# Kernel optimization log

Measured on AMD Instinct MI355X. Metric: run time of the kernel, lower is better.

Reference implementation:

```python
import jax, jax.numpy as jnp
import numpy as np

B, S, D, H = 4, 2048, 768, 12
HD = D // H
SCALE = HD ** -0.5


def setup_inputs() -> dict:
    key = jax.random.key(0)
    ks = jax.random.split(key, 10)
    inp = {
        "x": jax.random.normal(ks[0], (B, S, D), jnp.float32),
        "attn_mask": jax.random.normal(ks[1], (B, S), jnp.float32),
        "Wq": jax.random.normal(ks[2], (D, D), jnp.float32) * (D ** -0.5),
        "bq": jax.random.normal(ks[3], (D,), jnp.float32) * 0.02,
        "Wk": jax.random.normal(ks[4], (D, D), jnp.float32) * (D ** -0.5),
        "bk": jax.random.normal(ks[5], (D,), jnp.float32) * 0.02,
        "Wv": jax.random.normal(ks[6], (D, D), jnp.float32) * (D ** -0.5),
        "bv": jax.random.normal(ks[7], (D,), jnp.float32) * 0.02,
        "Wo": jax.random.normal(ks[8], (D, D), jnp.float32) * (D ** -0.5),
        "bo": jax.random.normal(ks[9], (D,), jnp.float32) * 0.02,
    }
    return inp


def _split_heads(e):
    # [B, S, D] -> [B, H, S, HD]
    return e.reshape(B, S, H, HD).transpose(0, 2, 1, 3)


def reference(x, attn_mask, Wq, bq, Wk, bk, Wv, bv, Wo, bo):
    q = _split_heads((x @ Wq + bq) * SCALE)          # [B,H,S,HD]
    k = _split_heads(x @ Wk + bk)                     # [B,H,S,HD]
    v = _split_heads(x @ Wv + bv)                     # [B,H,S,HD]
    scores = jnp.einsum('bhsd,bhtd->bhst', q, k)      # [B,H,S,S]
    scores = scores + attn_mask[:, None, None, :]     # additive mask over keys
    probs = jax.nn.softmax(scores, axis=-1)
    out = jnp.einsum('bhst,bhtd->bhsd', probs, v)     # [B,H,S,HD]
    out = out.transpose(0, 2, 1, 3).reshape(B, S, D)  # merge heads
    return out @ Wo + bo
```

## Files before the change

### kernel.cpp

```cpp
#include <hip/hip_runtime.h>
#include <cmath>

#define B_ 4
#define S_ 2048
#define D_ 768
#define H_ 12
#define HD_ 64
#define SCALE_ 0.125f
#define LOG2E_ 1.4426950408889634f
#define M_ 8192
#define NE_ 6291456ull

typedef unsigned short ushortT;
typedef unsigned int u32;
typedef __attribute__((ext_vector_type(8))) __bf16 bf16x8;
typedef __attribute__((ext_vector_type(4))) float f32x4;
typedef __attribute__((ext_vector_type(16))) float f32x16;

typedef __attribute__((address_space(1))) const void glb_cv;
typedef __attribute__((address_space(3))) void lds_v;

__device__ inline ushortT f2bf(float f) {
    return __builtin_bit_cast(ushortT, (__bf16)f);
}

__device__ inline u32 pk2bf(float a, float b) {
    return (u32)__builtin_bit_cast(ushortT, (__bf16)a)
         | ((u32)__builtin_bit_cast(ushortT, (__bf16)b) << 16);
}

__device__ inline void gload_lds16(const void* g, void* l) {
    __builtin_amdgcn_global_load_lds((glb_cv*)g, (lds_v*)l, 16, 0, 0);
}

__global__ __launch_bounds__(256)
void convert_f32_bf16(const float* __restrict__ in, ushortT* __restrict__ out)
{
    const size_t i = ((size_t)blockIdx.x * 256 + threadIdx.x) * 8;
    float4 a = *(const float4*)(in + i);
    float4 b = *(const float4*)(in + i + 4);
    union { ushortT u[8]; float4 f; } o;
    o.u[0] = f2bf(a.x); o.u[1] = f2bf(a.y); o.u[2] = f2bf(a.z); o.u[3] = f2bf(a.w);
    o.u[4] = f2bf(b.x); o.u[5] = f2bf(b.y); o.u[6] = f2bf(b.z); o.u[7] = f2bf(b.w);
    *(float4*)(out + i) = o.f;
}

__global__ __launch_bounds__(256)
void scale_mask(const float* __restrict__ in, float* __restrict__ outp)
{
    const int i = blockIdx.x * 256 + threadIdx.x;
    outp[i] = in[i] * LOG2E_;
}

__global__ __launch_bounds__(256)
void transpose_w(const float* __restrict__ W0, const float* __restrict__ W1,
                 const float* __restrict__ W2, const float* __restrict__ W3,
                 ushortT* __restrict__ wt4)
{
    const float* W = (blockIdx.z == 0) ? W0 : (blockIdx.z == 1) ? W1
                   : (blockIdx.z == 2) ? W2 : W3;
    ushortT* o = wt4 + (size_t)blockIdx.z * 768 * 768;
    __shared__ float T[64][65];
    const int tid = threadIdx.x;
    const int k0 = blockIdx.x * 64, n0 = blockIdx.y * 64;

    for (int t = tid; t < 1024; t += 256) {
        const int r = t >> 4, c4 = (t & 15) << 2;
        float4 v = *(const float4*)&W[(size_t)(k0 + r) * 768 + n0 + c4];
        T[r][c4 + 0] = v.x; T[r][c4 + 1] = v.y;
        T[r][c4 + 2] = v.z; T[r][c4 + 3] = v.w;
    }
    __syncthreads();
    for (int t = tid; t < 1024; t += 256) {
        const int r = t >> 4, c4 = (t & 15) << 2;
        union { ushortT u[4]; unsigned long long v; } ov;
        ov.u[0] = f2bf(T[c4 + 0][r]); ov.u[1] = f2bf(T[c4 + 1][r]);
        ov.u[2] = f2bf(T[c4 + 2][r]); ov.u[3] = f2bf(T[c4 + 3][r]);
        *(unsigned long long*)&o[(size_t)(n0 + r) * 768 + k0 + c4] = ov.v;
    }
}

__device__ inline void gemm_core_128x64(
    const ushortT* __restrict__ A, const ushortT* __restrict__ Bt,
    ushortT* As, ushortT* Bs, int m0, int n0, f32x4 acc[4][2])
{
    const int tid  = threadIdx.x;
    const int lane = tid & 63;
    const int wave = tid >> 6;
    const int lr = lane & 15, lg = lane >> 4;
    const int wr = wave >> 1, wc = wave & 1;

    #pragma unroll
    for (int mi = 0; mi < 4; ++mi)
        #pragma unroll
        for (int ni = 0; ni < 2; ++ni)
            acc[mi][ni] = (f32x4){0.f, 0.f, 0.f, 0.f};

    #pragma unroll 1
    for (int k0 = 0; k0 < 768; k0 += 64) {
        __syncthreads();
        #pragma unroll
        for (int it = 0; it < 4; ++it) {
            const int ci = it * 256 + tid;
            const int row = ci >> 3, c = ci & 7;
            const int sc = c ^ (row & 7);
            gload_lds16(A + (size_t)(m0 + row) * 768 + k0 + sc * 8,
                        As + (size_t)(it * 256 + wave * 64) * 8);
        }
        #pragma unroll
        for (int it = 0; it < 2; ++it) {
            const int ci = it * 256 + tid;
            const int row = ci >> 3, c = ci & 7;
            const int sc = c ^ (row & 7);
            gload_lds16(Bt + (size_t)(n0 + row) * 768 + k0 + sc * 8,
                        Bs + (size_t)(it * 256 + wave * 64) * 8);
        }
        __syncthreads();

        #pragma unroll
        for (int ks = 0; ks < 2; ++ks) {
            bf16x8 af[4], bfr[2];
            #pragma unroll
            for (int mi = 0; mi < 4; ++mi) {
                const int row = wr * 64 + mi * 16 + lr;
                const int ch = (ks * 4 + lg) ^ (row & 7);
                af[mi] = __builtin_bit_cast(bf16x8, *(const float4*)(As + row * 64 + ch * 8));
            }
            #pragma unroll
            for (int ni = 0; ni < 2; ++ni) {
                const int row = wc * 32 + ni * 16 + lr;
                const int ch = (ks * 4 + lg) ^ (row & 7);
                bfr[ni] = __builtin_bit_cast(bf16x8, *(const float4*)(Bs + row * 64 + ch * 8));
            }
            #pragma unroll
            for (int mi = 0; mi < 4; ++mi)
                #pragma unroll
                for (int ni = 0; ni < 2; ++ni)
                    acc[mi][ni] = __builtin_amdgcn_mfma_f32_16x16x32_bf16(
                        af[mi], bfr[ni], acc[mi][ni], 0, 0, 0);
        }
    }
}

__global__ __launch_bounds__(256)
void qkv_gemm(const ushortT* __restrict__ xb, const ushortT* __restrict__ wt4,
              const float* __restrict__ bq, const float* __restrict__ bk,
              const float* __restrict__ bv,
              ushortT* __restrict__ qb, ushortT* __restrict__ kb,
              ushortT* __restrict__ vtb)
{
    __shared__ __align__(16) ushortT As[128 * 64];
    __shared__ __align__(16) ushortT Bs[64 * 64];
    const int z = blockIdx.z;
    const ushortT* Wt = wt4 + (size_t)z * 768 * 768;
    const float* bias = (z == 0) ? bq : (z == 1) ? bk : bv;
    const float scale = (z == 0) ? (SCALE_ * LOG2E_) : 1.0f;

    const int m0 = blockIdx.x * 128, n0 = blockIdx.y * 64;
    f32x4 acc[4][2];
    gemm_core_128x64(xb, Wt, As, Bs, m0, n0, acc);

    const int tid = threadIdx.x;
    const int lane = tid & 63, wave = tid >> 6;
    const int lr = lane & 15, lg = lane >> 4;
    const int wr = wave >> 1, wc = wave & 1;
    const int h = n0 >> 6;

    if (z == 2) {
        #pragma unroll
        for (int ni = 0; ni < 2; ++ni) {
            const int nn = wc * 32 + ni * 16 + lr;
            const float bb = bias[n0 + nn];
            #pragma unroll
            for (int mi = 0; mi < 4; ++mi) {
                const int mb = m0 + wr * 64 + mi * 16 + lg * 4;
                const int b = mb >> 11, s = mb & 2047;
                ushort4 ov;
                ov.x = f2bf(acc[mi][ni][0] + bb);
                ov.y = f2bf(acc[mi][ni][1] + bb);
                ov.z = f2bf(acc[mi][ni][2] + bb);
                ov.w = f2bf(acc[mi][ni][3] + bb);
                *(ushort4*)&vtb[(((size_t)b * H_ + h) * HD_ + nn) * S_ + s] = ov;
            }
        }
    } else {
        ushortT* out = (z == 0) ? qb : kb;
        #pragma unroll
        for (int ni = 0; ni < 2; ++ni) {
            const int nn = wc * 32 + ni * 16 + lr;
            const float bb = bias[n0 + nn];
            #pragma unroll
            for (int mi = 0; mi < 4; ++mi) {
                #pragma unroll
                for (int j = 0; j < 4; ++j) {
                    const int m = m0 + wr * 64 + mi * 16 + lg * 4 + j;
                    const int b = m >> 11, s = m & 2047;
                    out[(((size_t)b * H_ + h) * S_ + s) * HD_ + nn] =
                        f2bf((acc[mi][ni][j] + bb) * scale);
                }
            }
        }
    }
}

__global__ __launch_bounds__(256)
void o_gemm(const ushortT* __restrict__ ab, const ushortT* __restrict__ wto,
            const float* __restrict__ bo, float* __restrict__ out)
{
    __shared__ __align__(16) ushortT As[128 * 64];
    __shared__ __align__(16) ushortT Bs[64 * 64];
    const int m0 = blockIdx.x * 128, n0 = blockIdx.y * 64;
    f32x4 acc[4][2];
    gemm_core_128x64(ab, wto, As, Bs, m0, n0, acc);

    const int tid = threadIdx.x;
    const int lane = tid & 63, wave = tid >> 6;
    const int lr = lane & 15, lg = lane >> 4;
    const int wr = wave >> 1, wc = wave & 1;

    #pragma unroll
    for (int ni = 0; ni < 2; ++ni) {
        const int n = n0 + wc * 32 + ni * 16 + lr;
        const float bb = bo[n];
        #pragma unroll
        for (int mi = 0; mi < 4; ++mi) {
            #pragma unroll
            for (int j = 0; j < 4; ++j) {
                const int m = m0 + wr * 64 + mi * 16 + lg * 4 + j;
                out[(size_t)m * 768 + n] = acc[mi][ni][j] + bb;
            }
        }
    }
}

__global__ __launch_bounds__(256, 3)
void attn_mfma(const ushortT* __restrict__ Q, const ushortT* __restrict__ K,
               const ushortT* __restrict__ Vt, const float* __restrict__ msc,
               ushortT* __restrict__ out)
{
    __shared__ __align__(16) ushortT Ks[2][64 * 64];
    __shared__ __align__(16) ushortT Vs[2][64 * 64];

    const int tid  = threadIdx.x;
    const int lane = tid & 63;
    const int wq   = tid >> 6;
    const int col  = lane & 31;
    const int hi   = lane >> 5;

    const int gid  = blockIdx.x;
    const int xcd  = gid & 7;
    const int w    = gid >> 3;
    const int bh_i = xcd * 6 + (w >> 4);
    const int q0   = (w & 15) * 128;
    const int b    = bh_i / H_;
    const int h    = bh_i % H_;
    const size_t bh = (size_t)bh_i;

    bf16x8 qf[4];
    {
        const ushortT* Qg = Q + (bh * S_ + q0 + wq * 32 + col) * HD_;
        #pragma unroll
        for (int ks = 0; ks < 4; ++ks)
            qf[ks] = __builtin_bit_cast(bf16x8,
                *(const float4*)(Qg + ks * 16 + hi * 8));
    }

    const ushortT* Kg = K  + bh * S_ * HD_;
    const ushortT* Vg = Vt + bh * HD_ * S_;
    const float*   mg = msc + (size_t)b * S_;

    const ushortT* ksrc[2];
    const ushortT* vsrc[2];
    #pragma unroll
    for (int it = 0; it < 2; ++it) {
        const int ci = it * 256 + tid;
        const int row = ci >> 3, c = ci & 7, sc = c ^ (row & 7);
        ksrc[it] = Kg + (size_t)row * HD_ + sc * 8;
        vsrc[it] = Vg + (size_t)row * S_ + sc * 8;
    }

    int ko[2][4], vo[2][4];
    #pragma unroll
    for (int kb2 = 0; kb2 < 2; ++kb2) {
        const int r = kb2 * 32 + col;
        #pragma unroll
        for (int ks = 0; ks < 4; ++ks)
            ko[kb2][ks] = r * 128 + (((2 * ks + hi) ^ (r & 7)) << 4);
    }
    #pragma unroll
    for (int hb = 0; hb < 2; ++hb) {
        const int r = hb * 32 + col;
        #pragma unroll
        for (int sg = 0; sg < 4; ++sg)
            vo[hb][sg] = r * 128 + (((2 * sg + hi) ^ (r & 7)) << 4);
    }

    bf16x8 onesA;
    #pragma unroll
    for (int i = 0; i < 8; ++i) onesA[i] = (__bf16)1.0f;

    f32x16 acc[2];
    f32x16 accl;
    #pragma unroll
    for (int hb = 0; hb < 2; ++hb)
        #pragma unroll
        for (int r = 0; r < 16; ++r) acc[hb][r] = 0.f;
    #pragma unroll
    for (int r = 0; r < 16; ++r) accl[r] = 0.f;

    auto stage = [&](int bsel) {
        #pragma unroll
        for (int it = 0; it < 2; ++it) {
            gload_lds16(ksrc[it], &Ks[bsel][(it * 256 + wq * 64) * 8]);
            ksrc[it] += 64 * HD_;
        }
        #pragma unroll
        for (int it = 0; it < 2; ++it) {
            gload_lds16(vsrc[it], &Vs[bsel][(it * 256 + wq * 64) * 8]);
            vsrc[it] += 64;
        }
    };

    stage(0);
    __syncthreads();

    for (int kt = 0; kt < S_ / 64; ++kt) {
        const int buf = kt & 1;
        if (kt + 1 < S_ / 64) stage(buf ^ 1);

        u32 bw[4][4];
        #pragma unroll
        for (int kb2 = 0; kb2 < 2; ++kb2) {
            f32x16 s;
            #pragma unroll
            for (int g = 0; g < 4; ++g) {
                float4 mv = *(const float4*)(mg + kt * 64 + kb2 * 32 + g * 8 + hi * 4);
                s[4 * g + 0] = mv.x;
                s[4 * g + 1] = mv.y;
                s[4 * g + 2] = mv.z;
                s[4 * g + 3] = mv.w;
            }

            __builtin_amdgcn_s_setprio(1);
            #pragma unroll
            for (int ks = 0; ks < 4; ++ks) {
                bf16x8 kf = __builtin_bit_cast(bf16x8,
                    *(const float4*)((const char*)&Ks[buf][0] + ko[kb2][ks]));
                s = __builtin_amdgcn_mfma_f32_32x32x16_bf16(
                    kf, qf[ks], s, 0, 0, 0);
            }
            __builtin_amdgcn_s_setprio(0);

            float p[16];
            #pragma unroll
            for (int r = 0; r < 16; ++r) p[r] = exp2f(s[r]);

            #pragma unroll
            for (int sl = 0; sl < 2; ++sl) {
                u32 u0 = pk2bf(p[8 * sl + 0], p[8 * sl + 1]);
                u32 u1 = pk2bf(p[8 * sl + 2], p[8 * sl + 3]);
                u32 v0 = pk2bf(p[8 * sl + 4], p[8 * sl + 5]);
                u32 v1 = pk2bf(p[8 * sl + 6], p[8 * sl + 7]);
                asm("v_permlane32_swap_b32 %0, %1" : "+v"(u0), "+v"(v0));
                asm("v_permlane32_swap_b32 %0, %1" : "+v"(u1), "+v"(v1));
                const int sg = kb2 * 2 + sl;
                bw[sg][0] = u0; bw[sg][1] = u1;
                bw[sg][2] = v0; bw[sg][3] = v1;
            }
        }

        __builtin_amdgcn_s_setprio(1);
        #pragma unroll
        for (int sg = 0; sg < 4; ++sg) {
            union { u32 w[4]; bf16x8 v; } pb;
            pb.w[0] = bw[sg][0]; pb.w[1] = bw[sg][1];
            pb.w[2] = bw[sg][2]; pb.w[3] = bw[sg][3];
            #pragma unroll
            for (int hb = 0; hb < 2; ++hb) {
                bf16x8 vf = __builtin_bit_cast(bf16x8,
                    *(const float4*)((const char*)&Vs[buf][0] + vo[hb][sg]));
                acc[hb] = __builtin_amdgcn_mfma_f32_32x32x16_bf16(
                    vf, pb.v, acc[hb], 0, 0, 0);
            }
            accl = __builtin_amdgcn_mfma_f32_32x32x16_bf16(
                onesA, pb.v, accl, 0, 0, 0);
        }
        __builtin_amdgcn_s_setprio(0);

        __syncthreads();
    }

    const float inv = 1.f / accl[0];
    const size_t row = (size_t)b * S_ + q0 + wq * 32 + col;
    #pragma unroll
    for (int hb = 0; hb < 2; ++hb) {
        #pragma unroll
        for (int t = 0; t < 4; ++t) {
            ushort4 ov;
            ov.x = f2bf(acc[hb][4 * t + 0] * inv);
            ov.y = f2bf(acc[hb][4 * t + 1] * inv);
            ov.z = f2bf(acc[hb][4 * t + 2] * inv);
            ov.w = f2bf(acc[hb][4 * t + 3] * inv);
            *(ushort4*)&out[row * D_ + h * HD_ + hb * 32 + t * 8 + hi * 4] = ov;
        }
    }
}

extern "C" void kernel_launch(void* const* d_in, const int* in_sizes, int n_in,
                              void* d_out, int out_size, void* d_ws, size_t ws_size,
                              hipStream_t stream)
{
    const float* x    = (const float*)d_in[0];
    const float* mask = (const float*)d_in[1];
    const float* Wq   = (const float*)d_in[2];
    const float* bq   = (const float*)d_in[3];
    const float* Wk   = (const float*)d_in[4];
    const float* bk   = (const float*)d_in[5];
    const float* Wv   = (const float*)d_in[6];
    const float* bv   = (const float*)d_in[7];
    const float* Wo   = (const float*)d_in[8];
    const float* bo   = (const float*)d_in[9];
    float* out = (float*)d_out;

    ushortT* xb  = (ushortT*)d_ws;
    ushortT* qb  = xb + NE_;
    ushortT* kb  = qb + NE_;
    ushortT* vtb = kb + NE_;
    ushortT* ab  = vtb + NE_;
    ushortT* wt4 = ab + NE_;
    float*   msc = (float*)(wt4 + (size_t)4 * 768 * 768);

    convert_f32_bf16<<<NE_ / 2048, 256, 0, stream>>>(x, xb);
    scale_mask<<<(B_ * S_) / 256, 256, 0, stream>>>(mask, msc);
    transpose_w<<<dim3(12, 12, 4), 256, 0, stream>>>(Wq, Wk, Wv, Wo, wt4);

    qkv_gemm<<<dim3(M_ / 128, 12, 3), 256, 0, stream>>>(
        xb, wt4, bq, bk, bv, qb, kb, vtb);

    attn_mfma<<<768, 256, 0, stream>>>(qb, kb, vtb, msc, ab);

    o_gemm<<<dim3(M_ / 128, 12), 256, 0, stream>>>(
        ab, wt4 + (size_t)3 * 768 * 768, bo, out);
}
```

Before: 171.2 us.

## Software-pipeline attention loop with triple-buffered K/V and QK-exp lookahead

Moves the attention loop to three LDS buffers for K/V and computes QK^T plus exp for tile kt+1 before the PV MFMAs of tile kt. The aim is to overlap the softmax exp and pack work with matrix-core work, and to give global-to-LDS loads two iterations of lead time. This raises LDS use from 32KB to 48KB per block, which may limit the 3-blocks-per-CU launch bound. It also keeps an extra set of packed P registers live, adding register pressure.

```diff
diff --git a/kernel.cpp b/kernel.cpp
--- a/kernel.cpp
+++ b/kernel.cpp
@@ -238,8 +238,8 @@
                const ushortT* __restrict__ Vt, const float* __restrict__ msc,
                ushortT* __restrict__ out)
 {
-    __shared__ __align__(16) ushortT Ks[2][64 * 64];
-    __shared__ __align__(16) ushortT Vs[2][64 * 64];
+    __shared__ __align__(16) ushortT Ks[3][64 * 64];
+    __shared__ __align__(16) ushortT Vs[3][64 * 64];
 
     const int tid  = threadIdx.x;
     const int lane = tid & 63;
@@ -321,14 +321,7 @@
         }
     };
 
-    stage(0);
-    __syncthreads();
-
-    for (int kt = 0; kt < S_ / 64; ++kt) {
-        const int buf = kt & 1;
-        if (kt + 1 < S_ / 64) stage(buf ^ 1);
-
-        u32 bw[4][4];
+    auto qkexp = [&](int kt, int bsel, u32 bwo[4][4]) {
         #pragma unroll
         for (int kb2 = 0; kb2 < 2; ++kb2) {
             f32x16 s;
@@ -340,14 +333,12 @@
                 s[4 * g + 2] = mv.z;
                 s[4 * g + 3] = mv.w;
             }
-
             __builtin_amdgcn_s_setprio(1);
             #pragma unroll
             for (int ks = 0; ks < 4; ++ks) {
                 bf16x8 kf = __builtin_bit_cast(bf16x8,
-                    *(const float4*)((const char*)&Ks[buf][0] + ko[kb2][ks]));
-                s = __builtin_amdgcn_mfma_f32_32x32x16_bf16(
-                    kf, qf[ks], s, 0, 0, 0);
+                    *(const float4*)((const char*)&Ks[bsel][0] + ko[kb2][ks]));
+                s = __builtin_amdgcn_mfma_f32_32x32x16_bf16(kf, qf[ks], s, 0, 0, 0);
             }
             __builtin_amdgcn_s_setprio(0);
 
@@ -364,21 +355,23 @@
                 asm("v_permlane32_swap_b32 %0, %1" : "+v"(u0), "+v"(v0));
                 asm("v_permlane32_swap_b32 %0, %1" : "+v"(u1), "+v"(v1));
                 const int sg = kb2 * 2 + sl;
-                bw[sg][0] = u0; bw[sg][1] = u1;
-                bw[sg][2] = v0; bw[sg][3] = v1;
-            }
-        }
-
+                bwo[sg][0] = u0; bwo[sg][1] = u1;
+                bwo[sg][2] = v0; bwo[sg][3] = v1;
+            }
+        }
+    };
+
+    auto pv = [&](int bsel, u32 bwi[4][4]) {
         __builtin_amdgcn_s_setprio(1);
         #pragma unroll
         for (int sg = 0; sg < 4; ++sg) {
             union { u32 w[4]; bf16x8 v; } pb;
-            pb.w[0] = bw[sg][0]; pb.w[1] = bw[sg][1];
-            pb.w[2] = bw[sg][2]; pb.w[3] = bw[sg][3];
+            pb.w[0] = bwi[sg][0]; pb.w[1] = bwi[sg][1];
+            pb.w[2] = bwi[sg][2]; pb.w[3] = bwi[sg][3];
             #pragma unroll
             for (int hb = 0; hb < 2; ++hb) {
                 bf16x8 vf = __builtin_bit_cast(bf16x8,
-                    *(const float4*)((const char*)&Vs[buf][0] + vo[hb][sg]));
+                    *(const float4*)((const char*)&Vs[bsel][0] + vo[hb][sg]));
                 acc[hb] = __builtin_amdgcn_mfma_f32_32x32x16_bf16(
                     vf, pb.v, acc[hb], 0, 0, 0);
             }
@@ -386,8 +379,27 @@
                 onesA, pb.v, accl, 0, 0, 0);
         }
         __builtin_amdgcn_s_setprio(0);
-
+    };
+
+    u32 bw[4][4], bwn[4][4];
+
+    stage(0);
+    __syncthreads();
+    stage(1);
+    qkexp(0, 0, bw);
+
+    int bp = 0, bq = 1, bs = 2;
+    #pragma unroll 1
+    for (int kt = 0; kt < S_ / 64; ++kt) {
         __syncthreads();
+        if (kt + 2 < S_ / 64) stage(bs);
+        if (kt + 1 < S_ / 64) qkexp(kt + 1, bq, bwn);
+        pv(bp, bw);
+        #pragma unroll
+        for (int i = 0; i < 4; ++i)
+            #pragma unroll
+            for (int j = 0; j < 4; ++j) bw[i][j] = bwn[i][j];
+        const int t2 = bp; bp = bq; bq = bs; bs = t2;
     }
 
     const float inv = 1.f / accl[0];
```

Result: no change. 173.0 us (+1.0%).

## Split attention over two key halves and add a combine kernel

Applied to the files above, without the earlier changes.

Each (batch, head, query-tile) attention block is split into two blocks, each covering half of the keys, so the grid doubles from 768 to 1536 blocks. Each block writes unnormalized bf16 partial outputs and its row sums. A new combine kernel adds the two halves and divides by the total row sum. This works without a running max because the kernel already accumulates plain exponential sums. The aim is more parallelism and shorter per-block loops, at the cost of an extra launch, extra global traffic for the partials, and an additional bf16 rounding of the unnormalized partials.

```diff
diff --git a/kernel.cpp b/kernel.cpp
--- a/kernel.cpp
+++ b/kernel.cpp
@@ -10,6 +10,7 @@
 #define LOG2E_ 1.4426950408889634f
 #define M_ 8192
 #define NE_ 6291456ull
+#define BHS_ 98304ull
 
 typedef unsigned short ushortT;
 typedef unsigned int u32;
@@ -22,6 +23,10 @@
 
 __device__ inline ushortT f2bf(float f) {
     return __builtin_bit_cast(ushortT, (__bf16)f);
+}
+
+__device__ inline float bf2f(ushortT u) {
+    return __builtin_bit_cast(float, (u32)u << 16);
 }
 
 __device__ inline u32 pk2bf(float a, float b) {
@@ -236,7 +241,7 @@
 __global__ __launch_bounds__(256, 3)
 void attn_mfma(const ushortT* __restrict__ Q, const ushortT* __restrict__ K,
                const ushortT* __restrict__ Vt, const float* __restrict__ msc,
-               ushortT* __restrict__ out)
+               ushortT* __restrict__ pn, float* __restrict__ pl)
 {
     __shared__ __align__(16) ushortT Ks[2][64 * 64];
     __shared__ __align__(16) ushortT Vs[2][64 * 64];
@@ -250,8 +255,10 @@
     const int gid  = blockIdx.x;
     const int xcd  = gid & 7;
     const int w    = gid >> 3;
-    const int bh_i = xcd * 6 + (w >> 4);
-    const int q0   = (w & 15) * 128;
+    const int bh_i = xcd * 6 + (w >> 5);
+    const int r5   = w & 31;
+    const int q0   = (r5 >> 1) * 128;
+    const int kh   = r5 & 1;
     const int b    = bh_i / H_;
     const int h    = bh_i % H_;
     const size_t bh = (size_t)bh_i;
@@ -265,9 +272,9 @@
                 *(const float4*)(Qg + ks * 16 + hi * 8));
     }
 
-    const ushortT* Kg = K  + bh * S_ * HD_;
-    const ushortT* Vg = Vt + bh * HD_ * S_;
-    const float*   mg = msc + (size_t)b * S_;
+    const ushortT* Kg = K  + bh * S_ * HD_ + (size_t)kh * 1024 * HD_;
+    const ushortT* Vg = Vt + bh * HD_ * S_ + (size_t)kh * 1024;
+    const float*   mg = msc + (size_t)b * S_ + (size_t)kh * 1024;
 
     const ushortT* ksrc[2];
     const ushortT* vsrc[2];
@@ -324,9 +331,9 @@
     stage(0);
     __syncthreads();
 
-    for (int kt = 0; kt < S_ / 64; ++kt) {
+    for (int kt = 0; kt < 16; ++kt) {
         const int buf = kt & 1;
-        if (kt + 1 < S_ / 64) stage(buf ^ 1);
+        if (kt + 1 < 16) stage(buf ^ 1);
 
         u32 bw[4][4];
         #pragma unroll
@@ -390,20 +397,45 @@
         __syncthreads();
     }
 
-    const float inv = 1.f / accl[0];
-    const size_t row = (size_t)b * S_ + q0 + wq * 32 + col;
+    ushortT* pnh = pn + (size_t)kh * NE_;
+    float*   plh = pl + (size_t)kh * BHS_;
+    const int q = q0 + wq * 32 + col;
+    const size_t row = (size_t)b * S_ + q;
+    plh[bh * S_ + q] = accl[0];
     #pragma unroll
     for (int hb = 0; hb < 2; ++hb) {
         #pragma unroll
         for (int t = 0; t < 4; ++t) {
             ushort4 ov;
-            ov.x = f2bf(acc[hb][4 * t + 0] * inv);
-            ov.y = f2bf(acc[hb][4 * t + 1] * inv);
-            ov.z = f2bf(acc[hb][4 * t + 2] * inv);
-            ov.w = f2bf(acc[hb][4 * t + 3] * inv);
-            *(ushort4*)&out[row * D_ + h * HD_ + hb * 32 + t * 8 + hi * 4] = ov;
-        }
-    }
+            ov.x = f2bf(acc[hb][4 * t + 0]);
+            ov.y = f2bf(acc[hb][4 * t + 1]);
+            ov.z = f2bf(acc[hb][4 * t + 2]);
+            ov.w = f2bf(acc[hb][4 * t + 3]);
+            *(ushort4*)&pnh[row * D_ + h * HD_ + hb * 32 + t * 8 + hi * 4] = ov;
+        }
+    }
+}
+
+__global__ __launch_bounds__(256)
+void combine(const ushortT* __restrict__ pn, const float* __restrict__ pl,
+             ushortT* __restrict__ ab)
+{
+    const size_t i8 = ((size_t)blockIdx.x * 256 + threadIdx.x) * 8;
+    const int d   = (int)(i8 % D_);
+    const size_t row = i8 / D_;
+    const int hh  = d >> 6;
+    const int b   = (int)(row >> 11);
+    const int s   = (int)(row & 2047);
+    const size_t li = ((size_t)b * H_ + hh) * S_ + s;
+    const float inv = 1.f / (pl[li] + pl[BHS_ + li]);
+
+    union { ushortT u[8]; float4 f; } a, c, o;
+    a.f = *(const float4*)(pn + i8);
+    c.f = *(const float4*)(pn + NE_ + i8);
+    #pragma unroll
+    for (int j = 0; j < 8; ++j)
+        o.u[j] = f2bf((bf2f(a.u[j]) + bf2f(c.u[j])) * inv);
+    *(float4*)(ab + i8) = o.f;
 }
 
 extern "C" void kernel_launch(void* const* d_in, const int* in_sizes, int n_in,
@@ -426,9 +458,11 @@
     ushortT* qb  = xb + NE_;
     ushortT* kb  = qb + NE_;
     ushortT* vtb = kb + NE_;
-    ushortT* ab  = vtb + NE_;
-    ushortT* wt4 = ab + NE_;
+    ushortT* pn  = vtb + NE_;
+    ushortT* wt4 = pn + 2 * NE_;
     float*   msc = (float*)(wt4 + (size_t)4 * 768 * 768);
+    float*   pl  = msc + (size_t)B_ * S_;
+    ushortT* ab  = xb;
 
     convert_f32_bf16<<<NE_ / 2048, 256, 0, stream>>>(x, xb);
     scale_mask<<<(B_ * S_) / 256, 256, 0, stream>>>(mask, msc);
@@ -437,7 +471,9 @@
     qkv_gemm<<<dim3(M_ / 128, 12, 3), 256, 0, stream>>>(
         xb, wt4, bq, bk, bv, qb, kb, vtb);
 
-    attn_mfma<<<768, 256, 0, stream>>>(qb, kb, vtb, msc, ab);
+    attn_mfma<<<1536, 256, 0, stream>>>(qb, kb, vtb, msc, pn, pl);
+
+    combine<<<NE_ / 2048, 256, 0, stream>>>(pn, pl, ab);
 
     o_gemm<<<dim3(M_ / 128, 12), 256, 0, stream>>>(
         ab, wt4 + (size_t)3 * 768 * 768, bo, out);
```

Result: slower. 175.8 us (+2.7%).

## Triple-buffer K/V tiles in attention with explicit vmcnt waits and raw barriers

Applied to the files above, without the earlier changes.

Moves the attention kernel's K/V LDS staging from double to triple buffering, prefetching two tiles ahead. Full __syncthreads is replaced by s_barrier plus hand-counted s_waitcnt vmcnt values, so global loads stay in flight across iterations instead of draining at every barrier. The mask loads are hoisted ahead of the stage call. LDS use grows by half, which may reduce occupancy at the requested 3 blocks per CU. The hardcoded vmcnt counts are fragile if the compiler emits a different number of memory ops.

```diff
diff --git a/kernel.cpp b/kernel.cpp
--- a/kernel.cpp
+++ b/kernel.cpp
@@ -238,8 +238,8 @@
                const ushortT* __restrict__ Vt, const float* __restrict__ msc,
                ushortT* __restrict__ out)
 {
-    __shared__ __align__(16) ushortT Ks[2][64 * 64];
-    __shared__ __align__(16) ushortT Vs[2][64 * 64];
+    __shared__ __align__(16) ushortT Ks[3][64 * 64];
+    __shared__ __align__(16) ushortT Vs[3][64 * 64];
 
     const int tid  = threadIdx.x;
     const int lane = tid & 63;
@@ -322,30 +322,47 @@
     };
 
     stage(0);
-    __syncthreads();
-
+    stage(1);
+
+    int bcur = 0, bstg = 2;
+    #pragma unroll 1
     for (int kt = 0; kt < S_ / 64; ++kt) {
-        const int buf = kt & 1;
-        if (kt + 1 < S_ / 64) stage(buf ^ 1);
-
-        u32 bw[4][4];
+        if (kt) __builtin_amdgcn_s_barrier();
+
+        f32x16 cin[2];
         #pragma unroll
         for (int kb2 = 0; kb2 < 2; ++kb2) {
-            f32x16 s;
             #pragma unroll
             for (int g = 0; g < 4; ++g) {
                 float4 mv = *(const float4*)(mg + kt * 64 + kb2 * 32 + g * 8 + hi * 4);
-                s[4 * g + 0] = mv.x;
-                s[4 * g + 1] = mv.y;
-                s[4 * g + 2] = mv.z;
-                s[4 * g + 3] = mv.w;
-            }
-
+                cin[kb2][4 * g + 0] = mv.x;
+                cin[kb2][4 * g + 1] = mv.y;
+                cin[kb2][4 * g + 2] = mv.z;
+                cin[kb2][4 * g + 3] = mv.w;
+            }
+        }
+        asm volatile("" ::: "memory");
+
+        if (kt + 2 < S_ / 64) stage(bstg);
+
+        if (kt <= S_ / 64 - 3)
+            asm volatile("s_waitcnt vmcnt(16)" ::: "memory");
+        else if (kt == S_ / 64 - 2)
+            asm volatile("s_waitcnt vmcnt(12)" ::: "memory");
+        else
+            asm volatile("s_waitcnt vmcnt(8)" ::: "memory");
+        __builtin_amdgcn_s_barrier();
+        __builtin_amdgcn_sched_barrier(0);
+
+        u32 bw[4][4];
+        #pragma unroll
+        for (int kb2 = 0; kb2 < 2; ++kb2) {
+            f32x16 s = cin[kb2];
             __builtin_amdgcn_s_setprio(1);
             #pragma unroll
             for (int ks = 0; ks < 4; ++ks) {
                 bf16x8 kf = __builtin_bit_cast(bf16x8,
-                    *(const float4*)((const char*)&Ks[buf][0] + ko[kb2][ks]));
+                    *(const float4*)((const char*)&Ks[bcur][0] + ko[kb2][ks]));
                 s = __builtin_amdgcn_mfma_f32_32x32x16_bf16(
                     kf, qf[ks], s, 0, 0, 0);
             }
@@ -378,7 +395,7 @@
             #pragma unroll
             for (int hb = 0; hb < 2; ++hb) {
                 bf16x8 vf = __builtin_bit_cast(bf16x8,
-                    *(const float4*)((const char*)&Vs[buf][0] + vo[hb][sg]));
+                    *(const float4*)((const char*)&Vs[bcur][0] + vo[hb][sg]));
                 acc[hb] = __builtin_amdgcn_mfma_f32_32x32x16_bf16(
                     vf, pb.v, acc[hb], 0, 0, 0);
             }
@@ -387,7 +404,8 @@
         }
         __builtin_amdgcn_s_setprio(0);
 
-        __syncthreads();
+        bcur = (bcur == 2) ? 0 : bcur + 1;
+        bstg = (bstg == 2) ? 0 : bstg + 1;
     }
 
     const float inv = 1.f / accl[0];
```

After: 174.1 us. About the same (+1.7%).
